# Performance work log

Measured on AMD Instinct MI355X. Metric: run time of the kernel, lower is better.

## Reference

```python
import jax, jax.numpy as jnp
import numpy as np

B, T, F, H, OUT, L = 4096, 336, 12, 50, 1, 3


def _lstm_layer(x_tbf, W_ih, W_hh, b_ih, b_hh):
    """PyTorch-semantics LSTM layer. x_tbf: [T,B,in]; returns [T,B,H]."""
    Hh = W_hh.shape[1]
    Bsz = x_tbf.shape[1]
    # precompute input projection for all timesteps: [T,B,4H]
    xz = jnp.einsum('tbf,gf->tbg', x_tbf, W_ih) + (b_ih + b_hh)

    def step(carry, xz_t):
        h, c = carry
        z = xz_t + h @ W_hh.T  # [B,4H]
        i, f, g, o = jnp.split(z, 4, axis=-1)  # PyTorch gate order i,f,g,o
        c = jax.nn.sigmoid(f) * c + jax.nn.sigmoid(i) * jnp.tanh(g)
        h = jax.nn.sigmoid(o) * jnp.tanh(c)
        return (h, c), h

    h0 = jnp.zeros((Bsz, Hh), x_tbf.dtype)
    c0 = jnp.zeros((Bsz, Hh), x_tbf.dtype)
    _, hs = jax.lax.scan(step, (h0, c0), xz)
    return hs


def setup_inputs() -> dict:
    key = jax.random.key(0)
    ks = jax.random.split(key, 16)
    s = 1.0 / np.sqrt(H)  # PyTorch LSTM init scale
    inp = {"x": jax.random.normal(ks[0], (B, T, F), dtype=jnp.float32)}
    in_sizes = [F, H, H]
    k = 1
    for l in range(L):
        inp[f"W_ih_{l}"] = jax.random.uniform(ks[k], (4 * H, in_sizes[l]), jnp.float32, -s, s); k += 1
        inp[f"W_hh_{l}"] = jax.random.uniform(ks[k], (4 * H, H), jnp.float32, -s, s); k += 1
        inp[f"b_ih_{l}"] = jax.random.uniform(ks[k], (4 * H,), jnp.float32, -s, s); k += 1
        inp[f"b_hh_{l}"] = jax.random.uniform(ks[k], (4 * H,), jnp.float32, -s, s); k += 1
    inp["W_lin"] = jax.random.uniform(ks[13], (OUT, H), jnp.float32, -s, s)
    inp["b_lin"] = jax.random.uniform(ks[14], (OUT,), jnp.float32, -s, s)
    return inp


def reference(x, W_ih_0, W_hh_0, b_ih_0, b_hh_0,
              W_ih_1, W_hh_1, b_ih_1, b_hh_1,
              W_ih_2, W_hh_2, b_ih_2, b_hh_2,
              W_lin, b_lin):
    h = jnp.transpose(x, (1, 0, 2))  # [T,B,F] time-major for scan
    params = [(W_ih_0, W_hh_0, b_ih_0, b_hh_0),
              (W_ih_1, W_hh_1, b_ih_1, b_hh_1),
              (W_ih_2, W_hh_2, b_ih_2, b_hh_2)]
    for W_ih, W_hh, bi, bh in params:
        h = _lstm_layer(h, W_ih, W_hh, bi, bh)  # [T,B,H]
    last = h[-1]  # out[:, -1, :] in batch_first layout
    return last @ W_lin.T + b_lin  # [B,OUT]
```

## Files before the change

### kernel.cpp

```cpp
#include <hip/hip_runtime.h>


#define Bsz 4096
#define Tt  336
#define BT  16
#define NTH 1024

typedef _Float16 half8 __attribute__((ext_vector_type(8)));
typedef float    floatx4 __attribute__((ext_vector_type(4)));

struct __align__(16) SMem {
  _Float16 act0[2][BT * 64];
  _Float16 act1[2][BT * 128];
  _Float16 act2[2][BT * 128];
};

__device__ __forceinline__ int offA0(int n, int L) {
  return n * 64 + ((((L >> 3) ^ n) & 7) << 3) + (L & 7);
}
__device__ __forceinline__ int offA12(int n, int L) {
  return n * 128 + ((((L >> 3) ^ n) & 15) << 3) + (L & 7);
}

__device__ __forceinline__ float lstm_cell(floatx4 z, float& c) {
  float ei = __builtin_amdgcn_exp2f(z[0]);
  float ef = __builtin_amdgcn_exp2f(z[1]);
  float eg = __builtin_amdgcn_exp2f(z[2]);
  float eo = __builtin_amdgcn_exp2f(z[3]);
  float ig = __builtin_amdgcn_rcpf(1.f + ei);
  float fg = __builtin_amdgcn_rcpf(1.f + ef);
  float rg = __builtin_amdgcn_rcpf(1.f + eg);
  float og = __builtin_amdgcn_rcpf(1.f + eo);
  float gg = 1.f - 2.f * rg;
  c = fg * c + ig * gg;
  float ec = __builtin_amdgcn_exp2f(2.885390082f * c);
  float rc = __builtin_amdgcn_rcpf(1.f + ec);
  return og * (1.f - 2.f * rc);
}

__device__ __forceinline__ half8 wfrag(const float* __restrict__ Wih,
                                       const float* __restrict__ Whh,
                                       int lenih, int bound, int R, int k0) {
  half8 r = {};
  int u = R >> 2, g = R & 3;
  float sc = (g == 2) ? 2.885390082f : -1.442695041f;
  if (u < 50) {
    int row = g * 50 + u;
#pragma unroll
    for (int j = 0; j < 8; ++j) {
      int k = k0 + j;
      float v = 0.f;
      if (k < bound)           v = Wih[row * lenih + k];
      else if (k < bound + 50) v = Whh[row * 50 + (k - bound)];
      r[j] = (_Float16)(sc * v);
    }
  }
  return r;
}

#define MFMA(a, b, acc) __builtin_amdgcn_mfma_f32_16x16x32_f16((a), (b), (acc), 0, 0, 0)

__global__ __launch_bounds__(NTH, 4)
void lstm_mfma_kernel(const float* __restrict__ x,
                      const float* __restrict__ Wih0, const float* __restrict__ Whh0,
                      const float* __restrict__ bih0, const float* __restrict__ bhh0,
                      const float* __restrict__ Wih1, const float* __restrict__ Whh1,
                      const float* __restrict__ bih1, const float* __restrict__ bhh1,
                      const float* __restrict__ Wih2, const float* __restrict__ Whh2,
                      const float* __restrict__ bih2, const float* __restrict__ bhh2,
                      const float* __restrict__ Wlin, const float* __restrict__ blin,
                      float* __restrict__ out) {
  __shared__ SMem sm;
  const int tid  = threadIdx.x;
  const int blk  = blockIdx.x;
  const int lane = tid & 63;
  const int w    = tid >> 6;
  const int n    = lane & 15;
  const int q    = lane >> 4;

  {
    int* zp = (int*)&sm;
    for (int i = tid; i < (int)(sizeof(SMem) / 4); i += NTH) zp[i] = 0;
  }

  int Lw, nc, mm3[3] = {0, 0, 0};
  switch (w) {
    case 0:  Lw = 0; nc = 3; mm3[0] = 0;  mm3[1] = 1;  mm3[2] = 2;  break;
    case 1:  Lw = 0; nc = 2; mm3[0] = 3;  mm3[1] = 4;               break;
    case 2:  Lw = 0; nc = 3; mm3[0] = 5;  mm3[1] = 6;  mm3[2] = 7;  break;
    case 3:  Lw = 0; nc = 2; mm3[0] = 8;  mm3[1] = 9;               break;
    case 4:  Lw = 1; nc = 2; mm3[0] = 0;  mm3[1] = 1;               break;
    case 5:  Lw = 1; nc = 3; mm3[0] = 2;  mm3[1] = 3;  mm3[2] = 4;  break;
    case 6:  Lw = 1; nc = 2; mm3[0] = 5;  mm3[1] = 6;               break;
    case 7:  Lw = 1; nc = 3; mm3[0] = 7;  mm3[1] = 8;  mm3[2] = 9;  break;
    case 8:  Lw = 2; nc = 3; mm3[0] = 0;  mm3[1] = 1;  mm3[2] = 2;  break;
    case 9:  Lw = 2; nc = 2; mm3[0] = 3;  mm3[1] = 4;               break;
    case 10: Lw = 2; nc = 2; mm3[0] = 5;  mm3[1] = 6;               break;
    case 11: Lw = 2; nc = 2; mm3[0] = 7;  mm3[1] = 8;               break;
    case 12: Lw = 2; nc = 2; mm3[0] = 9;  mm3[1] = 10;              break;
    case 13: Lw = 0; nc = 3; mm3[0] = 10; mm3[1] = 11; mm3[2] = 12; break;
    case 14: Lw = 1; nc = 3; mm3[0] = 10; mm3[1] = 11; mm3[2] = 12; break;
    default: Lw = 2; nc = 2; mm3[0] = 11; mm3[1] = 12;              break;
  }
  const float* Wih = (Lw == 0) ? Wih0 : ((Lw == 1) ? Wih1 : Wih2);
  const float* Whh = (Lw == 0) ? Whh0 : ((Lw == 1) ? Whh1 : Whh2);
  const float* bih = (Lw == 0) ? bih0 : ((Lw == 1) ? bih1 : bih2);
  const float* bhh = (Lw == 0) ? bhh0 : ((Lw == 1) ? bhh1 : bhh2);
  const int lenih = (Lw == 0) ? 12 : 50;
  const int nkc   = (Lw == 0) ? 2 : 4;

  half8  af[3][4];
  floatx4 bia[3];
  float  cst[3] = {0.f, 0.f, 0.f};
  int    woA[3], woB[3];
  bool   uokk[3];
#pragma unroll
  for (int i = 0; i < 3; ++i) {
    bia[i] = (floatx4){0, 0, 0, 0};
#pragma unroll
    for (int kc = 0; kc < 4; ++kc) af[i][kc] = (half8){};
    int m = mm3[i];
    int u = 4 * m + q;
    int uc = (u < 50) ? u : 49;
    uokk[i] = (i < nc) && (u < 50);
    if (Lw == 0) { woA[i] = offA0 (n, 12 + uc); woB[i] = offA12(n, uc); }
    else         { woA[i] = offA12(n, 50 + uc); woB[i] = offA12(n, uc); }
    if (i < nc) {
      int R = 16 * m + n;
#pragma unroll
      for (int kc = 0; kc < 4; ++kc)
        if (kc < nkc)
          af[i][kc] = wfrag(Wih, Whh, lenih, lenih, R, kc * 32 + q * 8);
      if (u < 50) {
#pragma unroll
        for (int g = 0; g < 4; ++g) {
          float sc = (g == 2) ? 2.885390082f : -1.442695041f;
          bia[i][g] = sc * (bih[g * 50 + u] + bhh[g * 50 + u]);
        }
      }
    }
  }

  const int ro0[2] = { offA0(n, q * 8), offA0(n, 32 + q * 8) };
  const int ro1[4] = { offA12(n, q * 8),      offA12(n, 32 + q * 8),
                       offA12(n, 64 + q * 8), offA12(n, 96 + q * 8) };

  const int sr = (tid < 192) ? tid / 12 : 0;
  const int sf = (tid < 192) ? tid - sr * 12 : 0;
  const int sxo = offA0(sr, sf);
  const float* xp = x + ((size_t)(blk * BT + sr) * Tt) * 12 + sf;
  float xnext = 0.f;

  __syncthreads();
  if (tid < 192) {
    sm.act0[0][sxo] = (_Float16)xp[0];
    xnext = xp[12];
  }
  __syncthreads();

#define TICK(p, TAU, CHK)                                                  \
  {                                                                        \
    if (Lw == 0) {                                                         \
      if (!(CHK) || (TAU) <= 335) {                                        \
        half8 b0 = *(const half8*)&sm.act0[p][ro0[0]];                     \
        half8 b1 = *(const half8*)&sm.act0[p][ro0[1]];                     \
        for (int i = 0; i < 3; ++i) if (i < nc) {                          \
          floatx4 z = bia[i];                                              \
          z = MFMA(af[i][0], b0, z);                                       \
          z = MFMA(af[i][1], b1, z);                                       \
          float h = lstm_cell(z, cst[i]);                                  \
          _Float16 hh = (_Float16)h;                                       \
          if (uokk[i]) { sm.act0[1 - (p)][woA[i]] = hh;                    \
                         sm.act1[1 - (p)][woB[i]] = hh; }                  \
        }                                                                  \
      }                                                                    \
    } else if (Lw == 1) {                                                  \
      if (!(CHK) || ((TAU) >= 1 && (TAU) <= 336)) {                        \
        half8 b0 = *(const half8*)&sm.act1[p][ro1[0]];                     \
        half8 b1 = *(const half8*)&sm.act1[p][ro1[1]];                     \
        half8 b2 = *(const half8*)&sm.act1[p][ro1[2]];                     \
        half8 b3 = *(const half8*)&sm.act1[p][ro1[3]];                     \
        for (int i = 0; i < 3; ++i) if (i < nc) {                          \
          floatx4 z = bia[i];                                              \
          z = MFMA(af[i][0], b0, z);                                       \
          z = MFMA(af[i][1], b1, z);                                       \
          z = MFMA(af[i][2], b2, z);                                       \
          z = MFMA(af[i][3], b3, z);                                       \
          float h = lstm_cell(z, cst[i]);                                  \
          _Float16 hh = (_Float16)h;                                       \
          if (uokk[i]) { sm.act1[1 - (p)][woA[i]] = hh;                    \
                         sm.act2[1 - (p)][woB[i]] = hh; }                  \
        }                                                                  \
      }                                                                    \
    } else {                                                               \
      if (!(CHK) || ((TAU) >= 2)) {                                        \
        half8 b0 = *(const half8*)&sm.act2[p][ro1[0]];                     \
        half8 b1 = *(const half8*)&sm.act2[p][ro1[1]];                     \
        half8 b2 = *(const half8*)&sm.act2[p][ro1[2]];                     \
        half8 b3 = *(const half8*)&sm.act2[p][ro1[3]];                     \
        for (int i = 0; i < 3; ++i) if (i < nc) {                          \
          floatx4 z = bia[i];                                              \
          z = MFMA(af[i][0], b0, z);                                       \
          z = MFMA(af[i][1], b1, z);                                       \
          z = MFMA(af[i][2], b2, z);                                       \
          z = MFMA(af[i][3], b3, z);                                       \
          float h = lstm_cell(z, cst[i]);                                  \
          if (uokk[i]) sm.act2[1 - (p)][woA[i]] = (_Float16)h;             \
        }                                                                  \
      }                                                                    \
    }                                                                      \
    if (tid < 192) {                                                       \
      if ((TAU) + 1 < Tt) sm.act0[1 - (p)][sxo] = (_Float16)xnext;         \
      xnext = ((TAU) + 2 < Tt) ? xp[((TAU) + 2) * 12] : 0.f;               \
    }                                                                      \
    __syncthreads();                                                       \
  }

  TICK(0, 0, 1)
  TICK(1, 1, 1)
#pragma unroll 1
  for (int t = 2; t < Tt; t += 2) {
    TICK(0, t, 0)
    TICK(1, t + 1, 0)
  }
  TICK(0, 336, 1)
  TICK(1, 337, 1)
#undef TICK

  if (tid < BT) {
    float s = blin[0];
    for (int uu = 0; uu < 50; ++uu)
      s += Wlin[uu] * (float)sm.act2[0][offA12(tid, 50 + uu)];
    out[blk * BT + tid] = s;
  }
}

extern "C" void kernel_launch(void* const* d_in, const int* in_sizes, int n_in,
                              void* d_out, int out_size, void* d_ws, size_t ws_size,
                              hipStream_t stream) {
  const float* x    = (const float*)d_in[0];
  const float* Wih0 = (const float*)d_in[1];
  const float* Whh0 = (const float*)d_in[2];
  const float* bih0 = (const float*)d_in[3];
  const float* bhh0 = (const float*)d_in[4];
  const float* Wih1 = (const float*)d_in[5];
  const float* Whh1 = (const float*)d_in[6];
  const float* bih1 = (const float*)d_in[7];
  const float* bhh1 = (const float*)d_in[8];
  const float* Wih2 = (const float*)d_in[9];
  const float* Whh2 = (const float*)d_in[10];
  const float* bih2 = (const float*)d_in[11];
  const float* bhh2 = (const float*)d_in[12];
  const float* Wlin = (const float*)d_in[13];
  const float* blin = (const float*)d_in[14];
  float* outp = (float*)d_out;

  dim3 grid(Bsz / BT);
  dim3 block(NTH);
  lstm_mfma_kernel<<<grid, block, 0, stream>>>(
      x, Wih0, Whh0, bih0, bhh0, Wih1, Whh1, bih1, bhh1,
      Wih2, Whh2, bih2, bhh2, Wlin, blin, outp);
}
```

Measured before the change: 405.4 us.

## Replace per-tick block barriers with fine-grained LDS progress counters between layer waves

Removes the __syncthreads at the end of every timestep tick. Each wave instead waits only on the specific producer and consumer waves it depends on, using per-wave read and write progress counters in shared memory with spin-wait and s_sleep. This lets layers advance with looser coupling and avoids full-block barriers. The cost is polling overhead and subtle memory-ordering risk with relaxed atomics and manual waitcnt.

```diff
diff --git a/kernel.cpp b/kernel.cpp
--- a/kernel.cpp
+++ b/kernel.cpp
@@ -58,7 +58,30 @@
   return r;
 }
 
+__device__ __forceinline__ void wait_all(int* prog, unsigned mask, int need, int lane) {
+  bool mine = (lane < 16) && ((mask >> lane) & 1u);
+  while (true) {
+    int v = mine ? __hip_atomic_load(&prog[lane & 15], __ATOMIC_RELAXED,
+                                     __HIP_MEMORY_SCOPE_WORKGROUP)
+                 : 0x7fffffff;
+    if (__all(v >= need)) break;
+    __builtin_amdgcn_s_sleep(1);
+  }
+  asm volatile("" ::: "memory");
+}
+__device__ __forceinline__ void store_prog(int* slot, int val, int lane) {
+  asm volatile("s_waitcnt lgkmcnt(0)" ::: "memory");
+  if (lane == 0)
+    __hip_atomic_store(slot, val, __ATOMIC_RELAXED, __HIP_MEMORY_SCOPE_WORKGROUP);
+}
+
 #define MFMA(a, b, acc) __builtin_amdgcn_mfma_f32_16x16x32_f16((a), (b), (acc), 0, 0, 0)
+
+#define MASK_L0   0x200Fu
+#define MASK_L1   0x40F0u
+#define MASK_L2   0x9F00u
+#define MASK_L01  0x60FFu
+#define MASK_L12  0xDFF0u
 
 __global__ __launch_bounds__(NTH, 4)
 void lstm_mfma_kernel(const float* __restrict__ x,
@@ -71,6 +94,8 @@
                       const float* __restrict__ Wlin, const float* __restrict__ blin,
                       float* __restrict__ out) {
   __shared__ SMem sm;
+  __shared__ int wrprog[16];
+  __shared__ int rdprog[16];
   const int tid  = threadIdx.x;
   const int blk  = blockIdx.x;
   const int lane = tid & 63;
@@ -82,6 +107,7 @@
     int* zp = (int*)&sm;
     for (int i = tid; i < (int)(sizeof(SMem) / 4); i += NTH) zp[i] = 0;
   }
+  if (tid < 16) { wrprog[tid] = 0; rdprog[tid] = 0; }
 
   int Lw, nc, mm3[3] = {0, 0, 0};
   switch (w) {
@@ -158,62 +184,90 @@
   }
   __syncthreads();
 
-#define TICK(p, TAU, CHK)                                                  \
-  {                                                                        \
-    if (Lw == 0) {                                                         \
-      if (!(CHK) || (TAU) <= 335) {                                        \
-        half8 b0 = *(const half8*)&sm.act0[p][ro0[0]];                     \
-        half8 b1 = *(const half8*)&sm.act0[p][ro0[1]];                     \
-        for (int i = 0; i < 3; ++i) if (i < nc) {                          \
-          floatx4 z = bia[i];                                              \
-          z = MFMA(af[i][0], b0, z);                                       \
-          z = MFMA(af[i][1], b1, z);                                       \
-          float h = lstm_cell(z, cst[i]);                                  \
-          _Float16 hh = (_Float16)h;                                       \
-          if (uokk[i]) { sm.act0[1 - (p)][woA[i]] = hh;                    \
-                         sm.act1[1 - (p)][woB[i]] = hh; }                  \
-        }                                                                  \
-      }                                                                    \
-    } else if (Lw == 1) {                                                  \
-      if (!(CHK) || ((TAU) >= 1 && (TAU) <= 336)) {                        \
-        half8 b0 = *(const half8*)&sm.act1[p][ro1[0]];                     \
-        half8 b1 = *(const half8*)&sm.act1[p][ro1[1]];                     \
-        half8 b2 = *(const half8*)&sm.act1[p][ro1[2]];                     \
-        half8 b3 = *(const half8*)&sm.act1[p][ro1[3]];                     \
-        for (int i = 0; i < 3; ++i) if (i < nc) {                          \
-          floatx4 z = bia[i];                                              \
-          z = MFMA(af[i][0], b0, z);                                       \
-          z = MFMA(af[i][1], b1, z);                                       \
-          z = MFMA(af[i][2], b2, z);                                       \
-          z = MFMA(af[i][3], b3, z);                                       \
-          float h = lstm_cell(z, cst[i]);                                  \
-          _Float16 hh = (_Float16)h;                                       \
-          if (uokk[i]) { sm.act1[1 - (p)][woA[i]] = hh;                    \
-                         sm.act2[1 - (p)][woB[i]] = hh; }                  \
-        }                                                                  \
-      }                                                                    \
-    } else {                                                               \
-      if (!(CHK) || ((TAU) >= 2)) {                                        \
-        half8 b0 = *(const half8*)&sm.act2[p][ro1[0]];                     \
-        half8 b1 = *(const half8*)&sm.act2[p][ro1[1]];                     \
-        half8 b2 = *(const half8*)&sm.act2[p][ro1[2]];                     \
-        half8 b3 = *(const half8*)&sm.act2[p][ro1[3]];                     \
-        for (int i = 0; i < 3; ++i) if (i < nc) {                          \
-          floatx4 z = bia[i];                                              \
-          z = MFMA(af[i][0], b0, z);                                       \
-          z = MFMA(af[i][1], b1, z);                                       \
-          z = MFMA(af[i][2], b2, z);                                       \
-          z = MFMA(af[i][3], b3, z);                                       \
-          float h = lstm_cell(z, cst[i]);                                  \
-          if (uokk[i]) sm.act2[1 - (p)][woA[i]] = (_Float16)h;             \
-        }                                                                  \
-      }                                                                    \
-    }                                                                      \
-    if (tid < 192) {                                                       \
-      if ((TAU) + 1 < Tt) sm.act0[1 - (p)][sxo] = (_Float16)xnext;         \
-      xnext = ((TAU) + 2 < Tt) ? xp[((TAU) + 2) * 12] : 0.f;               \
-    }                                                                      \
-    __syncthreads();                                                       \
+#define TICK(p, TAU, CHK)                                                   \
+  {                                                                         \
+    if (Lw == 0) {                                                          \
+      if (!(CHK) || (TAU) <= 335) {                                         \
+        wait_all(wrprog, MASK_L0, (TAU), lane);                             \
+        half8 b0 = *(const half8*)&sm.act0[p][ro0[0]];                      \
+        half8 b1 = *(const half8*)&sm.act0[p][ro0[1]];                      \
+        store_prog(&rdprog[w], (TAU) + 1, lane);                            \
+        float hv[3];                                                        \
+        for (int i = 0; i < 3; ++i) if (i < nc) {                           \
+          floatx4 z = bia[i];                                               \
+          z = MFMA(af[i][0], b0, z);                                        \
+          z = MFMA(af[i][1], b1, z);                                        \
+          hv[i] = lstm_cell(z, cst[i]);                                     \
+        }                                                                   \
+        wait_all(rdprog, MASK_L01, (TAU), lane);                            \
+        if (tid < 192 && (TAU) + 1 < Tt)                                    \
+          sm.act0[1 - (p)][sxo] = (_Float16)xnext;                          \
+        for (int i = 0; i < 3; ++i) if (uokk[i]) {                          \
+          _Float16 hh = (_Float16)hv[i];                                    \
+          sm.act0[1 - (p)][woA[i]] = hh;                                    \
+          sm.act1[1 - (p)][woB[i]] = hh;                                    \
+        }                                                                   \
+        store_prog(&wrprog[w], (TAU) + 1, lane);                            \
+        if (tid < 192)                                                      \
+          xnext = ((TAU) + 2 < Tt) ? xp[((TAU) + 2) * 12] : 0.f;            \
+      } else {                                                              \
+        store_prog(&rdprog[w], (TAU) + 1, lane);                            \
+        store_prog(&wrprog[w], (TAU) + 1, lane);                            \
+      }                                                                     \
+    } else if (Lw == 1) {                                                   \
+      if (!(CHK) || ((TAU) >= 1 && (TAU) <= 336)) {                         \
+        wait_all(wrprog, MASK_L01, (TAU), lane);                            \
+        half8 b0 = *(const half8*)&sm.act1[p][ro1[0]];                      \
+        half8 b1 = *(const half8*)&sm.act1[p][ro1[1]];                      \
+        half8 b2 = *(const half8*)&sm.act1[p][ro1[2]];                      \
+        half8 b3 = *(const half8*)&sm.act1[p][ro1[3]];                      \
+        store_prog(&rdprog[w], (TAU) + 1, lane);                            \
+        float hv[3];                                                        \
+        for (int i = 0; i < 3; ++i) if (i < nc) {                           \
+          floatx4 z = bia[i];                                               \
+          z = MFMA(af[i][0], b0, z);                                        \
+          z = MFMA(af[i][1], b1, z);                                        \
+          z = MFMA(af[i][2], b2, z);                                        \
+          z = MFMA(af[i][3], b3, z);                                        \
+          hv[i] = lstm_cell(z, cst[i]);                                     \
+        }                                                                   \
+        wait_all(rdprog, MASK_L12, (TAU), lane);                            \
+        for (int i = 0; i < 3; ++i) if (uokk[i]) {                          \
+          _Float16 hh = (_Float16)hv[i];                                    \
+          sm.act1[1 - (p)][woA[i]] = hh;                                    \
+          sm.act2[1 - (p)][woB[i]] = hh;                                    \
+        }                                                                   \
+        store_prog(&wrprog[w], (TAU) + 1, lane);                            \
+      } else {                                                              \
+        store_prog(&rdprog[w], (TAU) + 1, lane);                            \
+        store_prog(&wrprog[w], (TAU) + 1, lane);                            \
+      }                                                                     \
+    } else {                                                                \
+      if (!(CHK) || ((TAU) >= 2)) {                                         \
+        wait_all(wrprog, MASK_L12, (TAU), lane);                            \
+        half8 b0 = *(const half8*)&sm.act2[p][ro1[0]];                      \
+        half8 b1 = *(const half8*)&sm.act2[p][ro1[1]];                      \
+        half8 b2 = *(const half8*)&sm.act2[p][ro1[2]];                      \
+        half8 b3 = *(const half8*)&sm.act2[p][ro1[3]];                      \
+        store_prog(&rdprog[w], (TAU) + 1, lane);                            \
+        float hv[3];                                                        \
+        for (int i = 0; i < 3; ++i) if (i < nc) {                           \
+          floatx4 z = bia[i];                                               \
+          z = MFMA(af[i][0], b0, z);                                        \
+          z = MFMA(af[i][1], b1, z);                                        \
+          z = MFMA(af[i][2], b2, z);                                        \
+          z = MFMA(af[i][3], b3, z);                                        \
+          hv[i] = lstm_cell(z, cst[i]);                                     \
+        }                                                                   \
+        wait_all(rdprog, MASK_L2, (TAU), lane);                             \
+        for (int i = 0; i < 3; ++i) if (uokk[i])                            \
+          sm.act2[1 - (p)][woA[i]] = (_Float16)hv[i];                       \
+        store_prog(&wrprog[w], (TAU) + 1, lane);                            \
+      } else {                                                              \
+        store_prog(&rdprog[w], (TAU) + 1, lane);                            \
+        store_prog(&wrprog[w], (TAU) + 1, lane);                            \
+      }                                                                     \
+    }                                                                       \
   }
 
   TICK(0, 0, 1)
@@ -226,6 +280,8 @@
   TICK(0, 336, 1)
   TICK(1, 337, 1)
 #undef TICK
+
+  __syncthreads();
 
   if (tid < BT) {
     float s = blin[0];
```

After: 492.8 us. 21.6% more time.
